# Kernel optimization log

Hardware: AMD Instinct MI355X
Metric: run time of the kernel (lower is better)

Reference implementation:

```python
import jax, jax.numpy as jnp
import numpy as np

FILTERS = 64
NBITS = 4
NUE = 4
NSPU = 2
NST = NUE * NSPU           # 8 streams total
OUT_CH = NST * NBITS       # 32 output channels
NBS, NANT = 1, 16
CIN = NBS * NANT * 2 + NBS * NANT * NUE * NSPU * 2 + NUE * NSPU + 1  # 297


def hard_sigmoid(x):
    # Keras ConvLSTM2D default recurrent_activation
    return jnp.clip(0.2 * x + 0.5, 0.0, 1.0)


def conv2d(x, w):
    # x: [N,H,W,C], w: [kh,kw,Cin,Cout], SAME padding
    return jax.lax.conv_general_dilated(x, w, (1, 1), 'SAME',
                                        dimension_numbers=('NHWC', 'HWIO', 'NHWC'))


def convlstm2d(x, Wx, Wh, b):
    """Keras ConvLSTM2D (return_sequences=True), gate order i,f,c,o.
    x: [B,T,H,W,Cin] -> [B,T,H,W,F].
    Input-to-hidden convs are precomputed for all timesteps at once;
    only the cheap hidden-to-hidden conv is inside the scan."""
    B, T, H, W, Cin = x.shape
    F = Wh.shape[2]
    xz = conv2d(x.reshape(B * T, H, W, Cin), Wx).reshape(B, T, H, W, 4 * F) + b
    xz = jnp.moveaxis(xz, 1, 0)  # [T,B,H,W,4F]
    h0 = jnp.zeros((B, H, W, F), x.dtype)

    def step(carry, z_in):
        h, c = carry
        z = z_in + conv2d(h, Wh)
        zi, zf, zg, zo = jnp.split(z, 4, axis=-1)
        i = hard_sigmoid(zi)
        f = hard_sigmoid(zf)
        g = jnp.tanh(zg)
        o = hard_sigmoid(zo)
        c = f * c + i * g
        h = o * jnp.tanh(c)
        return (h, c), h

    _, hs = jax.lax.scan(step, (h0, h0), xz)
    return jnp.moveaxis(hs, 0, 1)  # [B,T,H,W,F]


def _lstm_params(key, cin, f, scale=0.05):
    k1, k2, k3 = jax.random.split(key, 3)
    Wx = jax.random.normal(k1, (3, 3, cin, 4 * f), jnp.float32) * scale
    Wh = jax.random.normal(k2, (3, 3, f, 4 * f), jnp.float32) * scale
    b = jax.random.normal(k3, (4 * f,), jnp.float32) * scale
    return Wx, Wh, b


def setup_inputs() -> dict:
    key = jax.random.key(0)
    ks = jax.random.split(key, 10)
    B, T, W = 2, 14, 1536
    inp = {
        'y_ri': jax.random.normal(ks[0], (B, NBS, NANT, T, W, 2), jnp.float32),
        'h_ri': jax.random.normal(ks[1], (B, NBS, NANT, NUE, NSPU, T, W, 2), jnp.float32),
        'err_var': jax.random.uniform(ks[2], (1, 1, 1, NUE, NSPU, T, W), jnp.float32),
        'no': jax.random.uniform(ks[3], (1,), jnp.float32),
    }
    inp['Wx_in'], inp['Wh_in'], inp['b_in'] = _lstm_params(ks[4], CIN, FILTERS)
    inp['Wx_r0'], inp['Wh_r0'], inp['b_r0'] = _lstm_params(ks[5], FILTERS, FILTERS)
    inp['Wx_r1'], inp['Wh_r1'], inp['b_r1'] = _lstm_params(ks[6], FILTERS, FILTERS)
    inp['Wx_out'], inp['Wh_out'], inp['b_out'] = _lstm_params(ks[7], FILTERS, OUT_CH)
    return inp


def _forward(y_ri, h_ri, err_var, no,
             Wx_in, Wh_in, b_in,
             Wx_r0, Wh_r0, b_r0,
             Wx_r1, Wh_r1, b_r1,
             Wx_out, Wh_out, b_out):
    B, nbs, nant, T, W, _ = y_ri.shape
    # y: [B,nbs,nant,T,W,2] -> [B,T,W,nbs*nant*2]
    y_feats = jnp.transpose(y_ri, (0, 3, 4, 1, 2, 5)).reshape(B, T, W, -1)
    # h: [B,nbs,nant,ue,spu,T,W,2] -> [B,T,W,nbs*nant*ue*spu*2]
    h_feats = jnp.transpose(h_ri, (0, 5, 6, 1, 2, 3, 4, 7)).reshape(B, T, W, -1)
    # err_var: [1,1,1,ue,spu,T,W] -> [B,T,W,ue*spu]
    ev = jnp.transpose(err_var[0, 0, 0], (2, 3, 0, 1)).reshape(1, T, W, NUE * NSPU)
    err_feats = jnp.broadcast_to(ev, (B, T, W, NUE * NSPU))
    no_feat = jnp.broadcast_to(no.reshape(1, 1, 1, 1), (B, T, W, 1))
    z = jnp.concatenate([y_feats, h_feats, err_feats, no_feat], axis=-1)
    z = z[:, :, :, None, :]  # [B,T,W,1,C]

    z = convlstm2d(z, Wx_in, Wh_in, b_in)
    # residual blocks (in_ch == filters, so identity skip)
    z = convlstm2d(z, Wx_r0, Wh_r0, b_r0) + z
    z = convlstm2d(z, Wx_r1, Wh_r1, b_r1) + z
    z = convlstm2d(z, Wx_out, Wh_out, b_out)

    z = z[:, :, :, 0, :]  # [B,T,W,OUT_CH]
    N = T * W
    z = z.reshape(B, N, NUE, NSPU, NBITS)
    z = jnp.transpose(z, (0, 2, 3, 1, 4))
    return z.reshape(B, NUE, NSPU, N * NBITS)


def reference(y_ri, h_ri, err_var, no,
              Wx_in, Wh_in, b_in,
              Wx_r0, Wh_r0, b_r0,
              Wx_r1, Wh_r1, b_r1,
              Wx_out, Wh_out, b_out):
    return _forward(y_ri, h_ri, err_var, no,
                    Wx_in, Wh_in, b_in,
                    Wx_r0, Wh_r0, b_r0,
                    Wx_r1, Wh_r1, b_r1,
                    Wx_out, Wh_out, b_out)
```

## Files before the change

### kernel.cpp

```cpp
#include <hip/hip_runtime.h>
#include <hip/hip_bf16.h>


#define BB   2
#define TT   14
#define LL   1536
#define LL2  1538
#define CINR 297
#define CP_IN 320
#define NSTRIP 128
#define OWN    12
#define OWN0   18
#define NBLK  (BB * NSTRIP)
#define WIN  48

typedef __attribute__((ext_vector_type(8))) short short8;
typedef __attribute__((ext_vector_type(4))) float floatx4;

static constexpr size_t U_WBIN_HI  = 0;
static constexpr size_t U_WBIN_LO  = 245760;
static constexpr size_t U_WBR0_HI  = 491520;
static constexpr size_t U_WBR0_LO  = 540672;
static constexpr size_t U_WBR1_HI  = 589824;
static constexpr size_t U_WBR1_LO  = 638976;
static constexpr size_t U_WBOUT_HI = 688128;
static constexpr size_t U_WBOUT_LO = 712704;
static constexpr size_t U_WHTIN    = 737280;
static constexpr size_t U_WHTR0    = 786432;
static constexpr size_t U_WHTR1    = 835584;
static constexpr size_t U_WHTOUT   = 884736;
static constexpr size_t OFF_BIN   = 448512;
static constexpr size_t OFF_BR0   = 448768;
static constexpr size_t OFF_BR1   = 449024;
static constexpr size_t OFF_BOUT  = 449280;
static constexpr size_t OFF_Z0HI  = 458752;
static constexpr size_t SZ_Z0PL   = 6890240;
static constexpr size_t OFF_Z0LO  = OFF_Z0HI + SZ_Z0PL;
static constexpr size_t OFF_XZ    = OFF_Z0LO + SZ_Z0PL;
static constexpr size_t SZ_XZ     = (size_t)BB*TT*LL*256;
static constexpr size_t OFF_SEQ   = OFF_Z0HI;
static constexpr size_t OFF_SEQHI = OFF_SEQ + (size_t)BB*TT*LL2*64;
static constexpr size_t OFF_SEQLO = OFF_SEQHI + (size_t)BB*TT*LL2*32;

__device__ __forceinline__ float hsig(float x) {
    return fminf(fmaxf(0.2f * x + 0.5f, 0.0f), 1.0f);
}
__device__ __forceinline__ float ftanh(float x) {
    float e = __expf(2.0f * x);
    return 1.0f - 2.0f / (e + 1.0f);
}
__device__ __forceinline__ unsigned short f2bf(float x) {
    unsigned int u = __builtin_bit_cast(unsigned int, x);
    u += 0x7fffu + ((u >> 16) & 1u);
    return (unsigned short)(u >> 16);
}
__device__ __forceinline__ float bf2f(unsigned short h) {
    unsigned int u = ((unsigned int)h) << 16;
    return __builtin_bit_cast(float, u);
}

__global__ __launch_bounds__(256)
void zero_pads_kernel(unsigned short* __restrict__ z0hi,
                      unsigned short* __restrict__ z0lo)
{
    int idx = blockIdx.x * 256 + threadIdx.x;
    const int NZ = BB * TT * 2 * CP_IN;
    if (idx < NZ) {
        int c = idx % CP_IN, r2 = idx / CP_IN;
        int p = r2 >> 1, e = r2 & 1;
        long long off = ((long long)p * LL2 + (e ? (LL2 - 1) : 0)) * CP_IN + c;
        z0hi[off] = 0; z0lo[off] = 0;
    }
}

__global__ __launch_bounds__(256)
void zero_seq_pads_kernel(unsigned short* __restrict__ seqhb,
                          unsigned short* __restrict__ seqlb)
{
    int idx = blockIdx.x * 256 + threadIdx.x;
    const int NS = BB * TT * 2 * 64;
    if (idx < NS) {
        int c = idx % 64, r2 = idx / 64;
        int p = r2 >> 1, e = r2 & 1;
        long long off = ((long long)p * LL2 + (e ? (LL2 - 1) : 0)) * 64 + c;
        seqhb[off] = 0; seqlb[off] = 0;
    }
}

__global__ __launch_bounds__(256)
void prep_weights_kernel(const float* wx_in, const float* wh_in, const float* b_in,
                         const float* wx_r0, const float* wh_r0, const float* b_r0,
                         const float* wx_r1, const float* wh_r1, const float* b_r1,
                         const float* wx_out, const float* wh_out, const float* b_out,
                         float* __restrict__ ws)
{
    int idx = blockIdx.x * 256 + threadIdx.x;
    unsigned short* u = (unsigned short*)ws;
    if (idx < 245760) {
        int j = idx & 7, lane = (idx >> 3) & 63, frag = idx >> 9;
        int g = frag & 15, rest = frag >> 4;
        int kh = rest % 3, cc = rest / 3;
        int mm = lane & 15, quad = lane >> 4;
        int n = g * 16 + mm;
        int ci = cc * 32 + quad * 8 + j;
        float v = 0.0f;
        if (ci < CINR)
            v = wx_in[((size_t)(kh * 3 + 1) * CINR + ci) * 256 + (n & 3) * 64 + (n >> 2)];
        unsigned short hi = f2bf(v);
        u[U_WBIN_HI + idx] = hi;
        u[U_WBIN_LO + idx] = f2bf(v - bf2f(hi));
        return;
    }
    idx -= 245760;
    if (idx < 49152) {
        int j = idx & 7, lane = (idx >> 3) & 63, frag = idx >> 9;
        int g = frag & 15, rest = frag >> 4;
        int kh = rest % 3, cc = rest / 3;
        int mm = lane & 15, quad = lane >> 4;
        int n = g * 16 + mm;
        int ci = cc * 32 + quad * 8 + j;
        float v = wx_r0[((size_t)(kh * 3 + 1) * 64 + ci) * 256 + (n & 3) * 64 + (n >> 2)];
        unsigned short hi = f2bf(v);
        u[U_WBR0_HI + idx] = hi;
        u[U_WBR0_LO + idx] = f2bf(v - bf2f(hi));
        return;
    }
    idx -= 49152;
    if (idx < 49152) {
        int j = idx & 7, lane = (idx >> 3) & 63, frag = idx >> 9;
        int g = frag & 15, rest = frag >> 4;
        int kh = rest % 3, cc = rest / 3;
        int mm = lane & 15, quad = lane >> 4;
        int n = g * 16 + mm;
        int ci = cc * 32 + quad * 8 + j;
        float v = wx_r1[((size_t)(kh * 3 + 1) * 64 + ci) * 256 + (n & 3) * 64 + (n >> 2)];
        unsigned short hi = f2bf(v);
        u[U_WBR1_HI + idx] = hi;
        u[U_WBR1_LO + idx] = f2bf(v - bf2f(hi));
        return;
    }
    idx -= 49152;
    if (idx < 24576) {
        int j = idx & 7, lane = (idx >> 3) & 63, frag = idx >> 9;
        int g = frag & 7, rest = frag >> 3;
        int kh = rest % 3, cc = rest / 3;
        int mm = lane & 15, quad = lane >> 4;
        int n = g * 16 + mm;
        int ci = cc * 32 + quad * 8 + j;
        float v = wx_out[((size_t)(kh * 3 + 1) * 64 + ci) * 128 + (n & 3) * 32 + (n >> 2)];
        unsigned short hi = f2bf(v);
        u[U_WBOUT_HI + idx] = hi;
        u[U_WBOUT_LO + idx] = f2bf(v - bf2f(hi));
        return;
    }
    idx -= 24576;
    if (idx < 49152) {
        int n = idx / 192, k = idx % 192, kh = k >> 6, ci = k & 63;
        u[U_WHTIN + idx] = f2bf(wh_in[((size_t)(kh * 3 + 1) * 64 + ci) * 256 + n]);
        return;
    }
    idx -= 49152;
    if (idx < 49152) {
        int n = idx / 192, k = idx % 192, kh = k >> 6, ci = k & 63;
        u[U_WHTR0 + idx] = f2bf(wh_r0[((size_t)(kh * 3 + 1) * 64 + ci) * 256 + n]);
        return;
    }
    idx -= 49152;
    if (idx < 49152) {
        int n = idx / 192, k = idx % 192, kh = k >> 6, ci = k & 63;
        u[U_WHTR1 + idx] = f2bf(wh_r1[((size_t)(kh * 3 + 1) * 64 + ci) * 256 + n]);
        return;
    }
    idx -= 49152;
    if (idx < 12288) {
        int n = idx / 96, k = idx % 96, kh = k / 32, ci = k % 32;
        u[U_WHTOUT + idx] = f2bf(wh_out[((size_t)(kh * 3 + 1) * 32 + ci) * 128 + n]);
        return;
    }
    idx -= 12288;
    if (idx < 256) { int f = idx >> 2, g = idx & 3; ws[OFF_BIN + idx] = b_in[g * 64 + f]; return; }
    idx -= 256;
    if (idx < 256) { int f = idx >> 2, g = idx & 3; ws[OFF_BR0 + idx] = b_r0[g * 64 + f]; return; }
    idx -= 256;
    if (idx < 256) { int f = idx >> 2, g = idx & 3; ws[OFF_BR1 + idx] = b_r1[g * 64 + f]; return; }
    idx -= 256;
    if (idx < 128) { int f = idx >> 2, g = idx & 3; ws[OFF_BOUT + idx] = b_out[g * 32 + f]; return; }
}

__global__ __launch_bounds__(256)
void build_features_kernel(const float* __restrict__ y,
                           const float* __restrict__ h,
                           const float* __restrict__ ev,
                           const float* __restrict__ no,
                           unsigned short* __restrict__ z0hi,
                           unsigned short* __restrict__ z0lo)
{
    long long idx = (long long)blockIdx.x * 256 + threadIdx.x;
    const long long total = (long long)BB * TT * LL * CP_IN;
    if (idx >= total) return;
    int c = (int)(idx % CP_IN);
    long long rest = idx / CP_IN;
    int l = (int)(rest % LL); rest /= LL;
    int t = (int)(rest % TT);
    int b = (int)(rest / TT);
    float v = 0.0f;
    if (c < 32) {
        int na = c >> 1, ri = c & 1;
        v = y[((((long long)b * 16 + na) * TT + t) * LL + l) * 2 + ri];
    } else if (c < 288) {
        int q = c - 32;
        int ri = q & 1, nspu = (q >> 1) & 1, nue = (q >> 2) & 3, na = q >> 4;
        v = h[((((((long long)b * 16 + na) * 4 + nue) * 2 + nspu) * TT + t) * LL + l) * 2 + ri];
    } else if (c < 296) {
        int q = c - 288; int nspu = q & 1, nue = q >> 1;
        v = ev[(((long long)(nue * 2 + nspu) * TT + t) * LL) + l];
    } else if (c == 296) {
        v = no[0];
    }
    const long long widx = (((long long)(b * TT + t)) * LL2 + (l + 1)) * CP_IN + c;
    unsigned short hi = f2bf(v);
    z0hi[widx] = hi;
    z0lo[widx] = f2bf(v - bf2f(hi));
}

template <int CP>
__global__ __launch_bounds__(256)
void xz_gemm_mfma_kernel(const unsigned short* __restrict__ Ahi,
                         const unsigned short* __restrict__ Alo,
                         const unsigned short* __restrict__ Bphi,
                         const unsigned short* __restrict__ Bplo,
                         const float* __restrict__ bias,
                         float* __restrict__ out, int Ncol)
{
    constexpr int NCm = CP / 64;
    __shared__ unsigned short AsHi[66 * 72], AsLo[66 * 72];
    const int tid  = threadIdx.x;
    const int lane = tid & 63;
    const int wv   = tid >> 6;
    const int m    = lane & 15;
    const int quad = lane >> 4;
    const int bt   = blockIdx.y;
    const int l0   = blockIdx.x * 64;
    const int n0   = blockIdx.z * 128;
    const int NG   = Ncol >> 4;
    const int gBase = (n0 >> 4) + wv;

    const int r0s = tid >> 3,        c0 = (tid & 7) * 8;
    const int r1s = (tid + 256) >> 3, c1 = (tid & 7) * 8;
    const int r2s = 64 + (tid >> 3),  c2 = (tid & 7) * 8;
    const long long aG0 = ((long long)bt * LL2 + l0 + r0s) * CP + c0;
    const long long aG1 = ((long long)bt * LL2 + l0 + r1s) * CP + c1;
    const long long aG2 = ((long long)bt * LL2 + l0 + r2s) * CP + c2;

    short8 g0h, g0l, g1h, g1l, g2h = (short8)0, g2l = (short8)0;

    g0h = *reinterpret_cast<const short8*>(&Ahi[aG0]);
    g0l = *reinterpret_cast<const short8*>(&Alo[aG0]);
    g1h = *reinterpret_cast<const short8*>(&Ahi[aG1]);
    g1l = *reinterpret_cast<const short8*>(&Alo[aG1]);
    if (tid < 16) {
        g2h = *reinterpret_cast<const short8*>(&Ahi[aG2]);
        g2l = *reinterpret_cast<const short8*>(&Alo[aG2]);
    }

    floatx4 acc[4][2];
#pragma unroll
    for (int i = 0; i < 4; i++)
#pragma unroll
        for (int j = 0; j < 2; j++) acc[i][j] = (floatx4){0.f, 0.f, 0.f, 0.f};

#pragma unroll 1
    for (int mc = 0; mc < NCm; ++mc) {
        __syncthreads();
        *reinterpret_cast<short8*>(&AsHi[r0s * 72 + c0]) = g0h;
        *reinterpret_cast<short8*>(&AsLo[r0s * 72 + c0]) = g0l;
        *reinterpret_cast<short8*>(&AsHi[r1s * 72 + c1]) = g1h;
        *reinterpret_cast<short8*>(&AsLo[r1s * 72 + c1]) = g1l;
        if (tid < 16) {
            *reinterpret_cast<short8*>(&AsHi[r2s * 72 + c2]) = g2h;
            *reinterpret_cast<short8*>(&AsLo[r2s * 72 + c2]) = g2l;
        }
        __syncthreads();
        if (mc + 1 < NCm) {
            const int co = (mc + 1) * 64;
            g0h = *reinterpret_cast<const short8*>(&Ahi[aG0 + co]);
            g0l = *reinterpret_cast<const short8*>(&Alo[aG0 + co]);
            g1h = *reinterpret_cast<const short8*>(&Ahi[aG1 + co]);
            g1l = *reinterpret_cast<const short8*>(&Alo[aG1 + co]);
            if (tid < 16) {
                g2h = *reinterpret_cast<const short8*>(&Ahi[aG2 + co]);
                g2l = *reinterpret_cast<const short8*>(&Alo[aG2 + co]);
            }
        }
#pragma unroll
        for (int sub = 0; sub < 2; ++sub) {
            const int cc = mc * 2 + sub;
            short8 bh[3][2], bl[3][2];
#pragma unroll
            for (int kh = 0; kh < 3; ++kh)
#pragma unroll
                for (int nt = 0; nt < 2; ++nt) {
                    const size_t off =
                        ((size_t)((cc * 3 + kh) * NG + gBase + nt * 4)) * 512 + lane * 8;
                    bh[kh][nt] = *reinterpret_cast<const short8*>(&Bphi[off]);
                    bl[kh][nt] = *reinterpret_cast<const short8*>(&Bplo[off]);
                }
#pragma unroll
            for (int kh = 0; kh < 3; ++kh) {
#pragma unroll
                for (int mt = 0; mt < 4; ++mt) {
                    const int aofs = (mt * 16 + m + kh) * 72 + sub * 32 + quad * 8;
                    const short8 ah = *reinterpret_cast<const short8*>(&AsHi[aofs]);
                    const short8 al = *reinterpret_cast<const short8*>(&AsLo[aofs]);
                    acc[mt][0] = __builtin_amdgcn_mfma_f32_16x16x32_bf16(al, bh[kh][0], acc[mt][0], 0, 0, 0);
                    acc[mt][0] = __builtin_amdgcn_mfma_f32_16x16x32_bf16(ah, bl[kh][0], acc[mt][0], 0, 0, 0);
                    acc[mt][0] = __builtin_amdgcn_mfma_f32_16x16x32_bf16(ah, bh[kh][0], acc[mt][0], 0, 0, 0);
                    acc[mt][1] = __builtin_amdgcn_mfma_f32_16x16x32_bf16(al, bh[kh][1], acc[mt][1], 0, 0, 0);
                    acc[mt][1] = __builtin_amdgcn_mfma_f32_16x16x32_bf16(ah, bl[kh][1], acc[mt][1], 0, 0, 0);
                    acc[mt][1] = __builtin_amdgcn_mfma_f32_16x16x32_bf16(ah, bh[kh][1], acc[mt][1], 0, 0, 0);
                }
            }
        }
    }

#pragma unroll
    for (int nt = 0; nt < 2; ++nt) {
        const int col = n0 + nt * 64 + wv * 16 + m;
        const float bv = bias[col];
#pragma unroll
        for (int mt = 0; mt < 4; ++mt) {
#pragma unroll
            for (int reg = 0; reg < 4; ++reg) {
                int l = l0 + mt * 16 + quad * 4 + reg;
                out[((size_t)bt * LL + l) * Ncol + col] = acc[mt][nt][reg] + bv;
            }
        }
    }
}

template <int F_, bool RESID, bool OUTW>
__global__ __launch_bounds__(64 * (F_ / 16))
void lstm_scan_kernel(const float* __restrict__ xz,
                      const unsigned short* __restrict__ WhT,
                      float* seq,
                      unsigned short* __restrict__ seqhb,
                      unsigned short* __restrict__ seqlb,
                      float* __restrict__ dout)
{
    constexpr int NW = F_ / 16;
    constexpr int NT = 64 * NW;
    constexpr int K  = 3 * F_;
    constexpr int KS = K / 32;
    constexpr int KH = KS / 3;
    constexpr int HP = F_ + 8;
    __shared__ unsigned short Hs[2][(WIN + 2) * HP];

    const int tid  = threadIdx.x;
    const int lane = tid & 63;
    const int wv   = tid >> 6;
    const int m    = lane & 15;
    const int quad = lane >> 4;
    const int blk  = blockIdx.x;
    const int b    = blk / NSTRIP;
    const int o0   = (blk % NSTRIP) * OWN;
    const int f    = wv * 16 + m;

    short8 bfr[4][KS];
#pragma unroll
    for (int g = 0; g < 4; g++)
#pragma unroll
        for (int ks = 0; ks < KS; ks++) {
            const int n  = g * F_ + f;
            const int k0 = ks * 32 + quad * 8;
            bfr[g][ks] = *reinterpret_cast<const short8*>(&WhT[(size_t)n * K + k0]);
        }

    for (int idx = tid; idx < (WIN + 2) * HP; idx += NT) {
        Hs[0][idx] = 0; Hs[1][idx] = 0;
    }
    __syncthreads();

    float c[3][4];
#pragma unroll
    for (int i = 0; i < 3; i++)
#pragma unroll
        for (int j = 0; j < 4; j++) c[i][j] = 0.0f;

    float4 xzA[3][4], xzB[3][4];
    float  rsA[4] = {0.f, 0.f, 0.f, 0.f}, rsB[4] = {0.f, 0.f, 0.f, 0.f};

    {
        const size_t btLn = (size_t)b * TT * LL;
#pragma unroll
        for (int mt = 0; mt < 3; ++mt)
#pragma unroll
            for (int reg = 0; reg < 4; ++reg) {
                const int w = mt * 16 + quad * 4 + reg;
                const int l = o0 - OWN0 + w;
                float4 v = make_float4(0.f, 0.f, 0.f, 0.f);
                if (l >= 0 && l < LL)
                    v = *reinterpret_cast<const float4*>(
                        &xz[(btLn + l) * (size_t)(4 * F_) + f * 4]);
                xzA[mt][reg] = v;
            }
        if (RESID) {
            const size_t btLPn = (size_t)b * TT * LL2;
#pragma unroll
            for (int reg = 0; reg < 4; ++reg) {
                const int w = 16 + quad * 4 + reg;
                float v = 0.f;
                if (w >= OWN0 && w < OWN0 + OWN)
                    v = seq[(btLPn + 1 + o0 + (w - OWN0)) * F_ + f];
                rsA[reg] = v;
            }
        }
    }

    int cur = 0;

#define SCAN_STEP(T, XZC, RSC, XZN, RSN)                                       \
    {                                                                          \
        const int t = (T);                                                     \
        if (t + 1 < TT) {                                                      \
            const size_t btLn = ((size_t)b * TT + (t + 1)) * LL;               \
            _Pragma("unroll")                                                  \
            for (int mt = 0; mt < 3; ++mt)                                     \
                _Pragma("unroll")                                              \
                for (int reg = 0; reg < 4; ++reg) {                            \
                    const int w = mt * 16 + quad * 4 + reg;                    \
                    const int l = o0 - OWN0 + w;                               \
                    float4 v = make_float4(0.f, 0.f, 0.f, 0.f);                \
                    if (l >= 0 && l < LL && w >= t + 1 && w < WIN - (t + 1))   \
                        v = *reinterpret_cast<const float4*>(                  \
                            &xz[(btLn + l) * (size_t)(4 * F_) + f * 4]);       \
                    XZN[mt][reg] = v;                                          \
                }                                                              \
            if (RESID) {                                                       \
                const size_t btLPn = ((size_t)b * TT + (t + 1)) * LL2;         \
                _Pragma("unroll")                                              \
                for (int reg = 0; reg < 4; ++reg) {                            \
                    const int w = 16 + quad * 4 + reg;                         \
                    float v = 0.f;                                             \
                    if (w >= OWN0 && w < OWN0 + OWN)                           \
                        v = seq[(btLPn + 1 + o0 + (w - OWN0)) * F_ + f];       \
                    RSN[reg] = v;                                              \
                }                                                              \
            }                                                                  \
        }                                                                      \
        const size_t btLP = ((size_t)b * TT + t) * LL2;                        \
        const int nxt = cur ^ 1;                                               \
        _Pragma("unroll")                                                      \
        for (int mt = 0; mt < 3; ++mt) {                                       \
            floatx4 zi = {0.f, 0.f, 0.f, 0.f};                                 \
            floatx4 zf = {0.f, 0.f, 0.f, 0.f};                                 \
            floatx4 zg = {0.f, 0.f, 0.f, 0.f};                                 \
            floatx4 zo = {0.f, 0.f, 0.f, 0.f};                                 \
            if (t > 0) {                                                       \
                _Pragma("unroll")                                              \
                for (int kh = 0; kh < 3; kh++) {                               \
                    _Pragma("unroll")                                          \
                    for (int hf = 0; hf < KH; hf++) {                          \
                        const short8 af = *reinterpret_cast<const short8*>(    \
                            &Hs[cur][(mt * 16 + m + kh) * HP + hf * 32 + quad * 8]); \
                        const int ks = kh * KH + hf;                           \
                        zi = __builtin_amdgcn_mfma_f32_16x16x32_bf16(af, bfr[0][ks], zi, 0, 0, 0); \
                        zf = __builtin_amdgcn_mfma_f32_16x16x32_bf16(af, bfr[1][ks], zf, 0, 0, 0); \
                        zg = __builtin_amdgcn_mfma_f32_16x16x32_bf16(af, bfr[2][ks], zg, 0, 0, 0); \
                        zo = __builtin_amdgcn_mfma_f32_16x16x32_bf16(af, bfr[3][ks], zo, 0, 0, 0); \
                    }                                                          \
                }                                                              \
            }                                                                  \
            _Pragma("unroll")                                                  \
            for (int reg = 0; reg < 4; ++reg) {                                \
                const int w = mt * 16 + quad * 4 + reg;                        \
                const int l = o0 - OWN0 + w;                                   \
                const bool valid = (l >= 0 && l < LL);                         \
                const float4 z4 = XZC[mt][reg];                                \
                const float ig = hsig(z4.x + zi[reg]);                         \
                const float fg = hsig(z4.y + zf[reg]);                         \
                const float gg = ftanh(z4.z + zg[reg]);                        \
                const float og = hsig(z4.w + zo[reg]);                         \
                float cn = fg * c[mt][reg] + ig * gg;                          \
                float hn = og * ftanh(cn);                                     \
                if (!valid) { cn = 0.0f; hn = 0.0f; }                          \
                c[mt][reg] = cn;                                               \
                Hs[nxt][(1 + w) * HP + f] = f2bf(hn);                          \
                if (w >= OWN0 && w < OWN0 + OWN) {                             \
                    if (OUTW) {                                                \
                        const int ue = f >> 3, spu = (f >> 2) & 1, bit = f & 3;\
                        const size_t n = (size_t)t * LL + l;                   \
                        dout[(((size_t)b * 4 + ue) * 2 + spu) * ((size_t)TT * LL * 4) \
                             + n * 4 + bit] = hn;                              \
                    } else {                                                   \
                        float v = hn;                                          \
                        if (RESID) v += RSC[reg];                              \
                        seq[(btLP + 1 + l) * F_ + f] = v;                      \
                        const unsigned short hi2 = f2bf(v);                    \
                        seqhb[(btLP + 1 + l) * F_ + f] = hi2;                  \
                        seqlb[(btLP + 1 + l) * F_ + f] = f2bf(v - bf2f(hi2));  \
                    }                                                          \
                }                                                              \
            }                                                                  \
        }                                                                      \
        __syncthreads();                         \
        cur = nxt;                                                             \
    }

#pragma unroll 1
    for (int t2 = 0; t2 < TT; t2 += 2) {
        SCAN_STEP(t2,     xzA, rsA, xzB, rsB)
        SCAN_STEP(t2 + 1, xzB, rsB, xzA, rsA)
    }
#undef SCAN_STEP
}

extern "C" void kernel_launch(void* const* d_in, const int* in_sizes, int n_in,
                              void* d_out, int out_size, void* d_ws, size_t ws_size,
                              hipStream_t stream)
{
    (void)in_sizes; (void)n_in; (void)out_size; (void)ws_size;
    const float* y_ri   = (const float*)d_in[0];
    const float* h_ri   = (const float*)d_in[1];
    const float* evar   = (const float*)d_in[2];
    const float* no     = (const float*)d_in[3];
    const float* wx_in  = (const float*)d_in[4];
    const float* wh_in  = (const float*)d_in[5];
    const float* b_in   = (const float*)d_in[6];
    const float* wx_r0  = (const float*)d_in[7];
    const float* wh_r0  = (const float*)d_in[8];
    const float* b_r0   = (const float*)d_in[9];
    const float* wx_r1  = (const float*)d_in[10];
    const float* wh_r1  = (const float*)d_in[11];
    const float* b_r1   = (const float*)d_in[12];
    const float* wx_out = (const float*)d_in[13];
    const float* wh_out = (const float*)d_in[14];
    const float* b_out  = (const float*)d_in[15];

    float* ws = (float*)d_ws;
    unsigned short* wu = (unsigned short*)d_ws;
    float* dout = (float*)d_out;

    unsigned short* z0hi = (unsigned short*)(ws + OFF_Z0HI);
    unsigned short* z0lo = (unsigned short*)(ws + OFF_Z0LO);
    float* xz    = ws + OFF_XZ;
    float* seq   = ws + OFF_SEQ;
    unsigned short* seqhb = (unsigned short*)(ws + OFF_SEQHI);
    unsigned short* seqlb = (unsigned short*)(ws + OFF_SEQLO);

    zero_pads_kernel<<<70, 256, 0, stream>>>(z0hi, z0lo);
    prep_weights_kernel<<<2068, 256, 0, stream>>>(
        wx_in, wh_in, b_in, wx_r0, wh_r0, b_r0,
        wx_r1, wh_r1, b_r1, wx_out, wh_out, b_out, ws);
    {
        long long total = (long long)BB * TT * LL * CP_IN;
        int blocks = (int)((total + 255) / 256);
        build_features_kernel<<<blocks, 256, 0, stream>>>(
            y_ri, h_ri, evar, no, z0hi, z0lo);
    }

    const dim3 gIn(LL / 64, BB * TT, 2);
    const dim3 gO (LL / 64, BB * TT, 1);

    xz_gemm_mfma_kernel<CP_IN><<<gIn, 256, 0, stream>>>(
        z0hi, z0lo, wu + U_WBIN_HI, wu + U_WBIN_LO, ws + OFF_BIN, xz, 256);
    zero_seq_pads_kernel<<<14, 256, 0, stream>>>(seqhb, seqlb);
    lstm_scan_kernel<64, false, false><<<NBLK, 256, 0, stream>>>(
        xz, wu + U_WHTIN, seq, seqhb, seqlb, nullptr);

    xz_gemm_mfma_kernel<64><<<gIn, 256, 0, stream>>>(
        seqhb, seqlb, wu + U_WBR0_HI, wu + U_WBR0_LO, ws + OFF_BR0, xz, 256);
    lstm_scan_kernel<64, true, false><<<NBLK, 256, 0, stream>>>(
        xz, wu + U_WHTR0, seq, seqhb, seqlb, nullptr);

    xz_gemm_mfma_kernel<64><<<gIn, 256, 0, stream>>>(
        seqhb, seqlb, wu + U_WBR1_HI, wu + U_WBR1_LO, ws + OFF_BR1, xz, 256);
    lstm_scan_kernel<64, true, false><<<NBLK, 256, 0, stream>>>(
        xz, wu + U_WHTR1, seq, seqhb, seqlb, nullptr);

    xz_gemm_mfma_kernel<64><<<gO, 256, 0, stream>>>(
        seqhb, seqlb, wu + U_WBOUT_HI, wu + U_WBOUT_LO, ws + OFF_BOUT, xz, 128);
    lstm_scan_kernel<32, false, true><<<NBLK, 128, 0, stream>>>(
        xz, wu + U_WHTOUT, nullptr, nullptr, nullptr, dout);
}
```

Measured before the change: 505.4 us.

## Widen owned strip to 16 columns, swizzle block order, lighten step barrier

```diff
diff --git a/kernel.cpp b/kernel.cpp
--- a/kernel.cpp
+++ b/kernel.cpp
@@ -8,9 +8,7 @@
 #define LL2  1538
 #define CINR 297
 #define CP_IN 320
-#define NSTRIP 128
-#define OWN    12
-#define OWN0   18
+#define NSTRIP 96
 #define NBLK  (BB * NSTRIP)
 #define WIN  48
 
@@ -360,9 +358,9 @@
     const int wv   = tid >> 6;
     const int m    = lane & 15;
     const int quad = lane >> 4;
-    const int blk  = blockIdx.x;
+    const int blk  = (blockIdx.x & 7) * (NBLK / 8) + (blockIdx.x >> 3);
     const int b    = blk / NSTRIP;
-    const int o0   = (blk % NSTRIP) * OWN;
+    const int o0   = (blk % NSTRIP) * 16;
     const int f    = wv * 16 + m;
 
     short8 bfr[4][KS];
@@ -390,28 +388,25 @@
     float  rsA[4] = {0.f, 0.f, 0.f, 0.f}, rsB[4] = {0.f, 0.f, 0.f, 0.f};
 
     {
-        const size_t btLn = (size_t)b * TT * LL;
+        const size_t btL0  = (size_t)b * TT * LL;
+        const size_t btLP0 = (size_t)b * TT * LL2;
 #pragma unroll
         for (int mt = 0; mt < 3; ++mt)
 #pragma unroll
             for (int reg = 0; reg < 4; ++reg) {
                 const int w = mt * 16 + quad * 4 + reg;
-                const int l = o0 - OWN0 + w;
+                const int l = o0 - 16 + w;
                 float4 v = make_float4(0.f, 0.f, 0.f, 0.f);
                 if (l >= 0 && l < LL)
                     v = *reinterpret_cast<const float4*>(
-                        &xz[(btLn + l) * (size_t)(4 * F_) + f * 4]);
+                        &xz[(btL0 + l) * (size_t)(4 * F_) + f * 4]);
                 xzA[mt][reg] = v;
             }
         if (RESID) {
-            const size_t btLPn = (size_t)b * TT * LL2;
 #pragma unroll
             for (int reg = 0; reg < 4; ++reg) {
-                const int w = 16 + quad * 4 + reg;
-                float v = 0.f;
-                if (w >= OWN0 && w < OWN0 + OWN)
-                    v = seq[(btLPn + 1 + o0 + (w - OWN0)) * F_ + f];
-                rsA[reg] = v;
+                const int l = o0 + quad * 4 + reg;
+                rsA[reg] = seq[(btLP0 + 1 + l) * F_ + f];
             }
         }
     }
@@ -421,14 +416,15 @@
 #define SCAN_STEP(T, XZC, RSC, XZN, RSN)                                       \
     {                                                                          \
         const int t = (T);                                                     \
-        if (t + 1 < TT) {                                                      \
-            const size_t btLn = ((size_t)b * TT + (t + 1)) * LL;               \
+        if (t + 1 < TT) {         \
+            const size_t btLn  = ((size_t)b * TT + (t + 1)) * LL;              \
+            const size_t btLPn = ((size_t)b * TT + (t + 1)) * LL2;             \
             _Pragma("unroll")                                                  \
             for (int mt = 0; mt < 3; ++mt)                                     \
                 _Pragma("unroll")                                              \
                 for (int reg = 0; reg < 4; ++reg) {                            \
                     const int w = mt * 16 + quad * 4 + reg;                    \
-                    const int l = o0 - OWN0 + w;                               \
+                    const int l = o0 - 16 + w;                                 \
                     float4 v = make_float4(0.f, 0.f, 0.f, 0.f);                \
                     if (l >= 0 && l < LL && w >= t + 1 && w < WIN - (t + 1))   \
                         v = *reinterpret_cast<const float4*>(                  \
@@ -436,17 +432,14 @@
                     XZN[mt][reg] = v;                                          \
                 }                                                              \
             if (RESID) {                                                       \
-                const size_t btLPn = ((size_t)b * TT + (t + 1)) * LL2;         \
                 _Pragma("unroll")                                              \
                 for (int reg = 0; reg < 4; ++reg) {                            \
-                    const int w = 16 + quad * 4 + reg;                         \
-                    float v = 0.f;                                             \
-                    if (w >= OWN0 && w < OWN0 + OWN)                           \
-                        v = seq[(btLPn + 1 + o0 + (w - OWN0)) * F_ + f];       \
-                    RSN[reg] = v;                                              \
+                    const int l = o0 + quad * 4 + reg;                         \
+                    RSN[reg] = seq[(btLPn + 1 + l) * F_ + f];                  \
                 }                                                              \
             }                                                                  \
         }                                                                      \
+        const size_t btL  = ((size_t)b * TT + t) * LL;                         \
         const size_t btLP = ((size_t)b * TT + t) * LL2;                        \
         const int nxt = cur ^ 1;                                               \
         _Pragma("unroll")                                                      \
@@ -473,7 +466,7 @@
             _Pragma("unroll")                                                  \
             for (int reg = 0; reg < 4; ++reg) {                                \
                 const int w = mt * 16 + quad * 4 + reg;                        \
-                const int l = o0 - OWN0 + w;                                   \
+                const int l = o0 - 16 + w;                                     \
                 const bool valid = (l >= 0 && l < LL);                         \
                 const float4 z4 = XZC[mt][reg];                                \
                 const float ig = hsig(z4.x + zi[reg]);                         \
@@ -485,7 +478,7 @@
                 if (!valid) { cn = 0.0f; hn = 0.0f; }                          \
                 c[mt][reg] = cn;                                               \
                 Hs[nxt][(1 + w) * HP + f] = f2bf(hn);                          \
-                if (w >= OWN0 && w < OWN0 + OWN) {                             \
+                if (w >= 16 && w < 32) {                                       \
                     if (OUTW) {                                                \
                         const int ue = f >> 3, spu = (f >> 2) & 1, bit = f & 3;\
                         const size_t n = (size_t)t * LL + l;                   \
@@ -502,7 +495,10 @@
                 }                                                              \
             }                                                                  \
         }                                                                      \
-        __syncthreads();                         \
+         \
+         \
+        asm volatile("s_waitcnt lgkmcnt(0)" ::: "memory");                     \
+        __builtin_amdgcn_s_barrier();                                          \
         cur = nxt;                                                             \
     }
 
```

Result: faster. 479.0 us (-5.2%).
